# Kernel optimization log

Hardware: AMD Instinct MI355X
Metric: run time of the kernel (lower is better)

Reference implementation:

```python
import jax, jax.numpy as jnp
import numpy as np

EPS = float(np.finfo(np.float32).eps)


def fake_quant_w(w):
    # per-output-channel symmetric int8 fake quant; w: (out, in)
    w_d = jax.lax.stop_gradient(w)
    max_abs = jnp.max(jnp.abs(w_d), axis=1, keepdims=True)
    scale = jnp.maximum(max_abs / 127.0, EPS)
    w_q = jnp.clip(jnp.round(w_d / scale), -127, 127)
    return w_q * scale


def woq_linear(x, w, b):
    return x @ fake_quant_w(w).T + b


def setup_inputs() -> dict:
    key = jax.random.key(0)
    ks = jax.random.split(key, 9)
    dim = 1024
    B, S = 2, 2048
    def wmat(k):
        return jax.random.normal(k, (dim, dim), dtype=jnp.float32) * (1.0 / np.sqrt(dim))
    def bvec(k):
        return jax.random.normal(k, (dim,), dtype=jnp.float32) * 0.01
    return {
        "x": jax.random.normal(ks[0], (B, S, dim), dtype=jnp.float32),
        "wq": wmat(ks[1]), "bq": bvec(ks[2]),
        "wk": wmat(ks[3]), "bk": bvec(ks[4]),
        "wv": wmat(ks[5]), "bv": bvec(ks[6]),
        "wp": wmat(ks[7]), "bp": bvec(ks[8]),
    }


def reference(x, wq, bq, wk, bk, wv, bv, wp, bp):
    B, S, C = x.shape
    H = 16
    D = C // H
    scale = D ** -0.5
    # QKV projections with fake-quantized weights -> (B, H, S, D)
    q = woq_linear(x, wq, bq).reshape(B, S, H, D).transpose(0, 2, 1, 3)
    k = woq_linear(x, wk, bk).reshape(B, S, H, D).transpose(0, 2, 1, 3)
    v = woq_linear(x, wv, bv).reshape(B, S, H, D).transpose(0, 2, 1, 3)
    attn = jnp.einsum("bhsd,bhtd->bhst", q, k) * scale  # (B,H,S,S)
    attn = jax.nn.softmax(attn, axis=-1)
    out = jnp.einsum("bhst,bhtd->bhsd", attn, v)
    out = out.transpose(0, 2, 1, 3).reshape(B, S, C)
    return woq_linear(out, wp, bp)
```

## Files before the change

kernel.cpp:

```cpp
#include <hip/hip_runtime.h>
#include <stdint.h>

typedef short bf16x8 __attribute__((ext_vector_type(8)));
typedef float f32x4 __attribute__((ext_vector_type(4)));
typedef uint16_t u16;
typedef uint32_t u32;
typedef u16 u16x4 __attribute__((ext_vector_type(4)));
typedef u32 u32x4 __attribute__((ext_vector_type(4)));

#define EPSF 1.1920929e-07f

static __device__ __forceinline__ u16 f2bf(float f) {
  union { float f; uint32_t u; } v; v.f = f;
  return (u16)((v.u + 0x7FFFu + ((v.u >> 16) & 1u)) >> 16);
}
static __device__ __forceinline__ float bf2f(u16 h) {
  union { uint32_t u; float f; } v; v.u = ((uint32_t)h) << 16;
  return v.f;
}
static __device__ __forceinline__ float exp2_fast(float x) {
  return __builtin_amdgcn_exp2f(x);
}
static __device__ __forceinline__ u32 cvt_pk_bf16(float lo, float hi) {
  u32 r;
  asm("v_cvt_pk_bf16_f32 %0, %1, %2" : "=v"(r) : "v"(lo), "v"(hi));
  return r;
}
static __device__ __forceinline__ void gload_lds16(const void* g, void* l) {
  __builtin_amdgcn_global_load_lds(
      (const __attribute__((address_space(1))) void*)g,
      (__attribute__((address_space(3))) void*)l, 16, 0, 0);
}
template <int N>
static __device__ __forceinline__ void vmwait() {
  asm volatile("s_waitcnt vmcnt(%0)" ::"i"(N) : "memory");
}

__global__ __launch_bounds__(256) void prep_kernel(
    const float* __restrict__ wq, const float* __restrict__ wk,
    const float* __restrict__ wv, const float* __restrict__ wp,
    const float* __restrict__ x,
    u16* __restrict__ wout, float* __restrict__ scales, u16* __restrict__ xb) {
  const int t = threadIdx.x;
  if (blockIdx.x < 4096) {
    const int row = blockIdx.x & 1023;
    const int mat = blockIdx.x >> 10;
    const float* W = (mat == 0) ? wq : (mat == 1) ? wk : (mat == 2) ? wv : wp;
    const float4 v = ((const float4*)(W + (size_t)row * 1024))[t];
    float m = fmaxf(fmaxf(fabsf(v.x), fabsf(v.y)), fmaxf(fabsf(v.z), fabsf(v.w)));
#pragma unroll
    for (int off = 1; off < 64; off <<= 1) m = fmaxf(m, __shfl_xor(m, off));
    __shared__ float red[4];
    if ((t & 63) == 0) red[t >> 6] = m;
    __syncthreads();
    m = fmaxf(fmaxf(red[0], red[1]), fmaxf(red[2], red[3]));
    const float scale = fmaxf(m / 127.0f, EPSF);
    float q0 = fminf(fmaxf(rintf(v.x / scale), -127.f), 127.f);
    float q1 = fminf(fmaxf(rintf(v.y / scale), -127.f), 127.f);
    float q2 = fminf(fmaxf(rintf(v.z / scale), -127.f), 127.f);
    float q3 = fminf(fmaxf(rintf(v.w / scale), -127.f), 127.f);
    u16x4 o; o.x = f2bf(q0); o.y = f2bf(q1); o.z = f2bf(q2); o.w = f2bf(q3);
    *(u16x4*)(wout + ((size_t)(mat * 1024 + row)) * 1024 + t * 4) = o;
    if (t == 0) scales[mat * 1024 + row] = scale;
  } else {
    const int i = (blockIdx.x - 4096) * 256 + t;
    const float4 v = ((const float4*)x)[i];
    u16x4 hv;
    hv.x = f2bf(v.x); hv.y = f2bf(v.y); hv.z = f2bf(v.z); hv.w = f2bf(v.w);
    *(u16x4*)(xb + (size_t)i * 4) = hv;
  }
}

template <int MODE, int MR, int NR, int NT, int KT, int LDA>
__global__ __launch_bounds__(512) void gemm_kernel(
    const u16* __restrict__ A, const u16* __restrict__ Bw,
    const float* __restrict__ scales, const float* __restrict__ b0,
    const float* __restrict__ b1, const float* __restrict__ b2,
    u16* __restrict__ qkv, float* __restrict__ outp) {
  constexpr int BM = 2 * MR * 16;
  constexpr int BN = 4 * NR * 16;
  constexpr int OPS = BM / 64 + BN / 64;
  __shared__ u16 As[2][BM * 64];
  __shared__ u16 Bs[2][BN * 64];
  const int tid = threadIdx.x;
  const int w = tid >> 6, l = tid & 63;
  const int per = gridDim.x >> 3;
  const int L = (blockIdx.x & 7) * per + (blockIdx.x >> 3);
  const int tile_n = (L % NT) * BN;
  const int tile_m = (L / NT) * BM;
  const int wm = w >> 2, wn = w & 3;
  const int l15 = l & 15, l4 = l >> 4;
  const int sw = l15 & 7;

  f32x4 acc[MR][NR];
  const f32x4 vzero = {0.f, 0.f, 0.f, 0.f};
#pragma unroll
  for (int m = 0; m < MR; ++m)
#pragma unroll
    for (int n = 0; n < NR; ++n) acc[m][n] = vzero;

  const int r8 = tid >> 3;
  const int g = tid & 7;
  const int gs = g ^ (r8 & 7);
  auto STAGE = [&](int slot, int j) {
    const int kb = j * 64;
    const int kbB = kb & 1023;
#pragma unroll
    for (int i = 0; i < BM / 64; ++i)
      gload_lds16(A + (size_t)(tile_m + i * 64 + r8) * LDA + kb + gs * 8,
                  &As[slot][(i * 64 + r8) * 64 + g * 8]);
#pragma unroll
    for (int i = 0; i < BN / 64; ++i)
      gload_lds16(Bw + (size_t)(tile_n + i * 64 + r8) * 1024 + kbB + gs * 8,
                  &Bs[slot][(i * 64 + r8) * 64 + g * 8]);
  };

  STAGE(0, 0);
  STAGE(1, 1);
  vmwait<OPS>();
  __builtin_amdgcn_s_barrier();

  for (int j = 0; j < KT; ++j) {
    const int cur = j & 1;
#pragma unroll
    for (int ks = 0; ks < 2; ++ks) {
      bf16x8 af[MR], bfv[NR];
      const int sg8 = ((ks * 4 + l4) ^ sw) * 8;
#pragma unroll
      for (int m = 0; m < MR; ++m)
        af[m] = *(const bf16x8*)(&As[cur][(wm * (MR * 16) + m * 16 + l15) * 64 + sg8]);
#pragma unroll
      for (int n = 0; n < NR; ++n)
        bfv[n] = *(const bf16x8*)(&Bs[cur][(wn * (NR * 16) + n * 16 + l15) * 64 + sg8]);
      __builtin_amdgcn_s_setprio(1);
#pragma unroll
      for (int m = 0; m < MR; ++m)
#pragma unroll
        for (int n = 0; n < NR; ++n)
          acc[m][n] = __builtin_amdgcn_mfma_f32_16x16x32_bf16(af[m], bfv[n], acc[m][n], 0, 0, 0);
      __builtin_amdgcn_s_setprio(0);
    }
    __builtin_amdgcn_s_barrier();
    if (j + 2 < KT) {
      STAGE(cur, j + 2);
      vmwait<OPS>();
    } else {
      vmwait<0>();
    }
    __builtin_amdgcn_s_barrier();
  }

#pragma unroll
  for (int m = 0; m < MR; ++m) {
#pragma unroll
    for (int n = 0; n < NR; ++n) {
      const int col = tile_n + wn * (NR * 16) + n * 16 + l15;
      const float sc = scales[col];
      if constexpr (MODE == 0) {
        const int mat = col >> 10, oo = col & 1023;
        const float* bias = (mat == 0) ? b0 : (mat == 1) ? b1 : b2;
        const float bb = bias[oo];
        const int hh = oo >> 6, dd = oo & 63;
        if (mat == 2) {
          const int rowm0 = tile_m + wm * (MR * 16) + m * 16 + l4 * 4;
          const int b = rowm0 >> 11, s = rowm0 & 2047;
          u16x4 pk;
#pragma unroll
          for (int jj = 0; jj < 4; ++jj) pk[jj] = f2bf(acc[m][n][jj] * sc + bb);
          const int kpos = (s & ~31) + ((s >> 2) & 3) * 8 + ((s >> 4) & 1) * 4;
          *(u16x4*)(qkv + (size_t)2 * 4194304 +
                    ((size_t)(b * 16 + hh) * 64 + dd) * 2048 + kpos) = pk;
        } else {
#pragma unroll
          for (int jj = 0; jj < 4; ++jj) {
            const int rowm = tile_m + wm * (MR * 16) + m * 16 + l4 * 4 + jj;
            const int b = rowm >> 11, s = rowm & 2047;
            float y = acc[m][n][jj] * sc + bb;
            if (mat == 0) y *= 0.18033688011112042f;
            qkv[(size_t)mat * 4194304 + ((size_t)(b * 16 + hh) * 2048 + s) * 64 + dd] = f2bf(y);
          }
        }
      } else {
        const float bb = b0[col];
#pragma unroll
        for (int jj = 0; jj < 4; ++jj) {
          const int rowm = tile_m + wm * (MR * 16) + m * 16 + l4 * 4 + jj;
          outp[(size_t)rowm * 1024 + col] = acc[m][n][jj] * sc + bb;
        }
      }
    }
  }
}

__global__ __launch_bounds__(512, 4) void attn_kernel(
    const u16* __restrict__ qg, const u16* __restrict__ kg,
    const u16* __restrict__ vtg, u16* __restrict__ po) {
  __shared__ u16 Kt[2][2][64 * 64];
  __shared__ u16 Vt[2][2][64 * 64];
  const int tid = threadIdx.x;
  const int w = tid >> 6, l = tid & 63;
  const int Lb = (blockIdx.x & 7) * 64 + (blockIdx.x >> 3);
  const int bh = Lb >> 4;
  const int qt = Lb & 15;
  const u16* qp = qg + (size_t)bh * 131072;
  const u16* kp = kg + (size_t)bh * 131072;
  const u16* vp = vtg + (size_t)bh * 131072;
  const int wg = w & 3, grp = w >> 2;
  const int qrow0 = qt * 128 + wg * 32;
  const int l15 = l & 15, l4 = l >> 4;
  const int sw = l15 & 7;

  const int sr = tid >> 3, sg = tid & 7;
  const int gsw = (sg ^ (sr & 7)) << 3;
  auto STAGE = [&](const int slot, const int j) {
    const int kA = j * 64, kB = 1024 + j * 64;
    gload_lds16(kp + (size_t)(kA + sr) * 64 + gsw, &Kt[slot][0][tid * 8]);
    gload_lds16(vp + (size_t)sr * 2048 + kA + gsw, &Vt[slot][0][tid * 8]);
    gload_lds16(kp + (size_t)(kB + sr) * 64 + gsw, &Kt[slot][1][tid * 8]);
    gload_lds16(vp + (size_t)sr * 2048 + kB + gsw, &Vt[slot][1][tid * 8]);
  };

  bf16x8 qfr[2][2];
#pragma unroll
  for (int dk = 0; dk < 2; ++dk)
#pragma unroll
    for (int qf = 0; qf < 2; ++qf)
      qfr[dk][qf] =
          *(const bf16x8*)(qp + (size_t)(qrow0 + qf * 16 + l15) * 64 + dk * 32 + l4 * 8);

  const f32x4 vzero = {0.f, 0.f, 0.f, 0.f};
  f32x4 O[4][2];
#pragma unroll
  for (int di = 0; di < 4; ++di)
#pragma unroll
    for (int qf = 0; qf < 2; ++qf) O[di][qf] = vzero;
  float lrun[2] = {0.f, 0.f};

  auto DO_ITER = [&](const int slot, const int j) {
    const u16* Kb = &Kt[slot][grp][0];
    const u16* Vb = &Vt[slot][grp][0];

    f32x4 sfr[2][4];
    {
      bf16x8 kf[4];
#pragma unroll
      for (int ki = 0; ki < 4; ++ki)
        kf[ki] = *(const bf16x8*)(Kb + (ki * 16 + l15) * 64 + ((l4 ^ sw) << 3));
      __builtin_amdgcn_s_setprio(1);
#pragma unroll
      for (int ki = 0; ki < 4; ++ki)
#pragma unroll
        for (int qf = 0; qf < 2; ++qf)
          sfr[qf][ki] = __builtin_amdgcn_mfma_f32_16x16x32_bf16(kf[ki], qfr[0][qf], vzero, 0, 0, 0);
      __builtin_amdgcn_s_setprio(0);
    }
    {
      bf16x8 kf[4];
#pragma unroll
      for (int ki = 0; ki < 4; ++ki)
        kf[ki] = *(const bf16x8*)(Kb + (ki * 16 + l15) * 64 + (((4 + l4) ^ sw) << 3));
      __builtin_amdgcn_s_setprio(1);
#pragma unroll
      for (int ki = 0; ki < 4; ++ki)
#pragma unroll
        for (int qf = 0; qf < 2; ++qf)
          sfr[qf][ki] = __builtin_amdgcn_mfma_f32_16x16x32_bf16(kf[ki], qfr[1][qf], sfr[qf][ki], 0, 0, 0);
      __builtin_amdgcn_s_setprio(0);
    }

    u32 pw[2][8];
#pragma unroll
    for (int qf = 0; qf < 2; ++qf) {
      float rs = 0.f;
#pragma unroll
      for (int ki = 0; ki < 4; ++ki) {
        const f32x4 s4 = sfr[qf][ki];
        const float p0 = exp2_fast(s4[0]);
        const float p1 = exp2_fast(s4[1]);
        const float p2 = exp2_fast(s4[2]);
        const float p3 = exp2_fast(s4[3]);
        rs += (p0 + p1) + (p2 + p3);
        pw[qf][ki * 2 + 0] = cvt_pk_bf16(p0, p1);
        pw[qf][ki * 2 + 1] = cvt_pk_bf16(p2, p3);
      }
      lrun[qf] += rs;
    }

#pragma unroll
    for (int kkl = 0; kkl < 2; ++kkl) {
      const u32x4 t0 = {pw[0][kkl * 4 + 0], pw[0][kkl * 4 + 1],
                        pw[0][kkl * 4 + 2], pw[0][kkl * 4 + 3]};
      const u32x4 t1 = {pw[1][kkl * 4 + 0], pw[1][kkl * 4 + 1],
                        pw[1][kkl * 4 + 2], pw[1][kkl * 4 + 3]};
      const bf16x8 pf0 = __builtin_bit_cast(bf16x8, t0);
      const bf16x8 pf1 = __builtin_bit_cast(bf16x8, t1);
      bf16x8 vf[4];
#pragma unroll
      for (int di = 0; di < 4; ++di)
        vf[di] = *(const bf16x8*)(Vb + (di * 16 + l15) * 64 +
                                  (((kkl * 4 + l4) ^ sw) << 3));
      __builtin_amdgcn_s_setprio(1);
#pragma unroll
      for (int di = 0; di < 4; ++di) {
        O[di][0] = __builtin_amdgcn_mfma_f32_16x16x32_bf16(pf0, vf[di], O[di][0], 0, 0, 0);
        O[di][1] = __builtin_amdgcn_mfma_f32_16x16x32_bf16(pf1, vf[di], O[di][1], 0, 0, 0);
      }
      __builtin_amdgcn_s_setprio(0);
    }

    __builtin_amdgcn_s_barrier();
    if (j + 2 < 16) {
      STAGE(slot, j + 2);
      vmwait<4>();
    } else {
      vmwait<0>();
    }
    __builtin_amdgcn_s_barrier();
  };

  STAGE(0, 0);
  STAGE(1, 1);
  vmwait<4>();
  __builtin_amdgcn_s_barrier();

  for (int jp = 0; jp < 8; ++jp) {
    DO_ITER(0, jp * 2);
    DO_ITER(1, jp * 2 + 1);
  }

  float* Osh = (float*)&Kt[0][0][0];
  float* lsh = (float*)&Vt[0][0][0];
  if (grp == 1) {
    float* ob = Osh + (0 * 4 + wg) * 1024;
#pragma unroll
    for (int di = 0; di < 4; ++di)
#pragma unroll
      for (int jj = 0; jj < 4; ++jj)
        ob[(l4 * 4 + jj) * 64 + di * 16 + l15] = O[di][0][jj];
    lsh[(0 * 4 + wg) * 64 + l] = lrun[0];
  } else {
    float* ob = Osh + (1 * 4 + wg) * 1024;
#pragma unroll
    for (int di = 0; di < 4; ++di)
#pragma unroll
      for (int jj = 0; jj < 4; ++jj)
        ob[(l4 * 4 + jj) * 64 + di * 16 + l15] = O[di][1][jj];
    lsh[(1 * 4 + wg) * 64 + l] = lrun[1];
  }
  __syncthreads();
  const int b = bh >> 4, hh = bh & 15;
  if (grp == 0) {
    const float* obr = Osh + (0 * 4 + wg) * 1024;
    float lt = lrun[0] + lsh[(0 * 4 + wg) * 64 + l];
    lt += __shfl_xor(lt, 16);
    lt += __shfl_xor(lt, 32);
    float lq[4];
#pragma unroll
    for (int jj = 0; jj < 4; ++jj)
      lq[jj] = __builtin_amdgcn_rcpf(__shfl(lt, l4 * 4 + jj));
#pragma unroll
    for (int di = 0; di < 4; ++di)
#pragma unroll
      for (int jj = 0; jj < 4; ++jj) {
        const float oval =
            (O[di][0][jj] + obr[(l4 * 4 + jj) * 64 + di * 16 + l15]) * lq[jj];
        const int srw = qrow0 + l4 * 4 + jj;
        const int c = hh * 64 + di * 16 + l15;
        po[((size_t)(b * 2048 + srw)) * 1024 + c] = f2bf(oval);
      }
  } else {
    const float* obr = Osh + (1 * 4 + wg) * 1024;
    float lt = lrun[1] + lsh[(1 * 4 + wg) * 64 + l];
    lt += __shfl_xor(lt, 16);
    lt += __shfl_xor(lt, 32);
    float lq[4];
#pragma unroll
    for (int jj = 0; jj < 4; ++jj)
      lq[jj] = __builtin_amdgcn_rcpf(__shfl(lt, l4 * 4 + jj));
#pragma unroll
    for (int di = 0; di < 4; ++di)
#pragma unroll
      for (int jj = 0; jj < 4; ++jj) {
        const float oval =
            (O[di][1][jj] + obr[(l4 * 4 + jj) * 64 + di * 16 + l15]) * lq[jj];
        const int srw = qrow0 + 16 + l4 * 4 + jj;
        const int c = hh * 64 + di * 16 + l15;
        po[((size_t)(b * 2048 + srw)) * 1024 + c] = f2bf(oval);
      }
  }
}

extern "C" void kernel_launch(void* const* d_in, const int* in_sizes, int n_in,
                              void* d_out, int out_size, void* d_ws, size_t ws_size,
                              hipStream_t stream) {
  (void)in_sizes; (void)n_in; (void)out_size; (void)ws_size;
  const float* x  = (const float*)d_in[0];
  const float* wq = (const float*)d_in[1];
  const float* bq = (const float*)d_in[2];
  const float* wk = (const float*)d_in[3];
  const float* bk = (const float*)d_in[4];
  const float* wv = (const float*)d_in[5];
  const float* bv = (const float*)d_in[6];
  const float* wp = (const float*)d_in[7];
  const float* bp = (const float*)d_in[8];

  char* ws = (char*)d_ws;
  u16*   wquant = (u16*)ws;
  float* scales = (float*)(ws + 8388608);
  u16*   xb     = (u16*)(ws + 8404992);
  u16*   po     = xb;
  u16*   qkv    = (u16*)(ws + 25182208);

  prep_kernel<<<dim3(8192), dim3(256), 0, stream>>>(
      wq, wk, wv, wp, x, wquant, scales, xb);
  gemm_kernel<0, 4, 3, 16, 16, 1024><<<dim3(512), dim3(512), 0, stream>>>(
      xb, wquant, scales, bq, bk, bv, qkv, nullptr);
  attn_kernel<<<dim3(512), dim3(512), 0, stream>>>(
      qkv, qkv + 4194304, qkv + 8388608, po);
  gemm_kernel<1, 2, 2, 8, 16, 1024><<<dim3(512), dim3(512), 0, stream>>>(
      po, wquant + 3145728, scales + 3072, bp, nullptr, nullptr, nullptr, (float*)d_out);
}
```

Measured before the change: 96.08 us.

## Add dedicated QKV GEMM kernel with 256x192 tiles and split-phase MFMA scheduling

Replaces the templated QKV projection GEMM (128x192 tiles, 512 blocks) with a dedicated kernel using 256x192 tiles and 256 blocks, so each block reuses more staged data per K step. The inner loop splits each k-substep into two halves with barriers and priority hints around MFMA bursts, and unrolls the double-buffer slots. Fewer blocks than CUs (256 on mi355x) and higher register pressure from 24 accumulators per wave may lower occupancy and leave hardware idle.

```diff
diff --git a/kernel.cpp b/kernel.cpp
--- a/kernel.cpp
+++ b/kernel.cpp
@@ -71,12 +71,126 @@
   }
 }
 
-template <int MODE, int MR, int NR, int NT, int KT, int LDA>
+__global__ __launch_bounds__(512, 2) void qkv_kernel(
+    const u16* __restrict__ A, const u16* __restrict__ Bw,
+    const float* __restrict__ scales, const float* __restrict__ b0,
+    const float* __restrict__ b1, const float* __restrict__ b2,
+    u16* __restrict__ qkv) {
+  __shared__ u16 As[2][256 * 64];
+  __shared__ u16 Bs[2][192 * 64];
+  const int tid = threadIdx.x;
+  const int w = tid >> 6, l = tid & 63;
+  const int L = (blockIdx.x & 7) * 32 + (blockIdx.x >> 3);
+  const int tile_n = (L & 15) * 192;
+  const int tile_m = (L >> 4) * 256;
+  const int wm = w >> 2, wn = w & 3;
+  const int l15 = l & 15, l4 = l >> 4;
+  const int sw = l15 & 7;
+
+  f32x4 acc[8][3];
+  const f32x4 vzero = {0.f, 0.f, 0.f, 0.f};
+#pragma unroll
+  for (int m = 0; m < 8; ++m)
+#pragma unroll
+    for (int n = 0; n < 3; ++n) acc[m][n] = vzero;
+
+  const int r8 = tid >> 3, g = tid & 7;
+  const int gs = g ^ (r8 & 7);
+  auto STAGE = [&](const int slot, const int j) {
+    const int kb = j * 64;
+#pragma unroll
+    for (int i = 0; i < 4; ++i)
+      gload_lds16(A + (size_t)(tile_m + i * 64 + r8) * 1024 + kb + gs * 8,
+                  &As[slot][(i * 64 + r8) * 64 + g * 8]);
+#pragma unroll
+    for (int i = 0; i < 3; ++i)
+      gload_lds16(Bw + (size_t)(tile_n + i * 64 + r8) * 1024 + kb + gs * 8,
+                  &Bs[slot][(i * 64 + r8) * 64 + g * 8]);
+  };
+
+  STAGE(0, 0);
+  STAGE(1, 1);
+  vmwait<7>();
+  __builtin_amdgcn_s_barrier();
+
+  auto KSTEP = [&](const int s, const int j) {
+#pragma unroll
+    for (int ks = 0; ks < 2; ++ks) {
+      bf16x8 bfv[3];
+      const int sg8 = ((ks * 4 + l4) ^ sw) << 3;
+#pragma unroll
+      for (int n = 0; n < 3; ++n)
+        bfv[n] = *(const bf16x8*)(&Bs[s][(wn * 48 + n * 16 + l15) * 64 + sg8]);
+#pragma unroll
+      for (int mh = 0; mh < 2; ++mh) {
+        bf16x8 af[4];
+#pragma unroll
+        for (int m4 = 0; m4 < 4; ++m4)
+          af[m4] = *(const bf16x8*)(&As[s][(wm * 128 + mh * 64 + m4 * 16 + l15) * 64 + sg8]);
+        __builtin_amdgcn_s_barrier();
+        __builtin_amdgcn_s_setprio(1);
+#pragma unroll
+        for (int m4 = 0; m4 < 4; ++m4)
+#pragma unroll
+          for (int n = 0; n < 3; ++n)
+            acc[mh * 4 + m4][n] = __builtin_amdgcn_mfma_f32_16x16x32_bf16(
+                af[m4], bfv[n], acc[mh * 4 + m4][n], 0, 0, 0);
+        __builtin_amdgcn_s_setprio(0);
+        __builtin_amdgcn_s_barrier();
+      }
+    }
+    if (j + 2 < 16) {
+      STAGE(s, j + 2);
+      vmwait<7>();
+    } else {
+      vmwait<0>();
+    }
+    __builtin_amdgcn_s_barrier();
+  };
+
+  for (int jp = 0; jp < 8; ++jp) {
+    KSTEP(0, jp * 2);
+    KSTEP(1, jp * 2 + 1);
+  }
+
+#pragma unroll
+  for (int m = 0; m < 8; ++m) {
+#pragma unroll
+    for (int n = 0; n < 3; ++n) {
+      const int col = tile_n + wn * 48 + n * 16 + l15;
+      const float sc = scales[col];
+      const int mat = col >> 10, oo = col & 1023;
+      const float* bias = (mat == 0) ? b0 : (mat == 1) ? b1 : b2;
+      const float bb = bias[oo];
+      const int hh = oo >> 6, dd = oo & 63;
+      if (mat == 2) {
+        const int rowm0 = tile_m + wm * 128 + m * 16 + l4 * 4;
+        const int b = rowm0 >> 11, s = rowm0 & 2047;
+        u16x4 pk;
+#pragma unroll
+        for (int jj = 0; jj < 4; ++jj) pk[jj] = f2bf(acc[m][n][jj] * sc + bb);
+        const int kpos = (s & ~31) + ((s >> 2) & 3) * 8 + ((s >> 4) & 1) * 4;
+        *(u16x4*)(qkv + (size_t)2 * 4194304 +
+                  ((size_t)(b * 16 + hh) * 64 + dd) * 2048 + kpos) = pk;
+      } else {
+#pragma unroll
+        for (int jj = 0; jj < 4; ++jj) {
+          const int rowm = tile_m + wm * 128 + m * 16 + l4 * 4 + jj;
+          const int b = rowm >> 11, s = rowm & 2047;
+          float y = acc[m][n][jj] * sc + bb;
+          if (mat == 0) y *= 0.18033688011112042f;
+          qkv[(size_t)mat * 4194304 + ((size_t)(b * 16 + hh) * 2048 + s) * 64 + dd] = f2bf(y);
+        }
+      }
+    }
+  }
+}
+
+template <int MR, int NR, int NT, int KT, int LDA>
 __global__ __launch_bounds__(512) void gemm_kernel(
     const u16* __restrict__ A, const u16* __restrict__ Bw,
     const float* __restrict__ scales, const float* __restrict__ b0,
-    const float* __restrict__ b1, const float* __restrict__ b2,
-    u16* __restrict__ qkv, float* __restrict__ outp) {
+    float* __restrict__ outp) {
   constexpr int BM = 2 * MR * 16;
   constexpr int BN = 4 * NR * 16;
   constexpr int OPS = BM / 64 + BN / 64;
@@ -156,37 +270,11 @@
     for (int n = 0; n < NR; ++n) {
       const int col = tile_n + wn * (NR * 16) + n * 16 + l15;
       const float sc = scales[col];
-      if constexpr (MODE == 0) {
-        const int mat = col >> 10, oo = col & 1023;
-        const float* bias = (mat == 0) ? b0 : (mat == 1) ? b1 : b2;
-        const float bb = bias[oo];
-        const int hh = oo >> 6, dd = oo & 63;
-        if (mat == 2) {
-          const int rowm0 = tile_m + wm * (MR * 16) + m * 16 + l4 * 4;
-          const int b = rowm0 >> 11, s = rowm0 & 2047;
-          u16x4 pk;
-#pragma unroll
-          for (int jj = 0; jj < 4; ++jj) pk[jj] = f2bf(acc[m][n][jj] * sc + bb);
-          const int kpos = (s & ~31) + ((s >> 2) & 3) * 8 + ((s >> 4) & 1) * 4;
-          *(u16x4*)(qkv + (size_t)2 * 4194304 +
-                    ((size_t)(b * 16 + hh) * 64 + dd) * 2048 + kpos) = pk;
-        } else {
-#pragma unroll
-          for (int jj = 0; jj < 4; ++jj) {
-            const int rowm = tile_m + wm * (MR * 16) + m * 16 + l4 * 4 + jj;
-            const int b = rowm >> 11, s = rowm & 2047;
-            float y = acc[m][n][jj] * sc + bb;
-            if (mat == 0) y *= 0.18033688011112042f;
-            qkv[(size_t)mat * 4194304 + ((size_t)(b * 16 + hh) * 2048 + s) * 64 + dd] = f2bf(y);
-          }
-        }
-      } else {
-        const float bb = b0[col];
-#pragma unroll
-        for (int jj = 0; jj < 4; ++jj) {
-          const int rowm = tile_m + wm * (MR * 16) + m * 16 + l4 * 4 + jj;
-          outp[(size_t)rowm * 1024 + col] = acc[m][n][jj] * sc + bb;
-        }
+      const float bb = b0[col];
+#pragma unroll
+      for (int jj = 0; jj < 4; ++jj) {
+        const int rowm = tile_m + wm * (MR * 16) + m * 16 + l4 * 4 + jj;
+        outp[(size_t)rowm * 1024 + col] = acc[m][n][jj] * sc + bb;
       }
     }
   }
@@ -413,10 +501,10 @@
 
   prep_kernel<<<dim3(8192), dim3(256), 0, stream>>>(
       wq, wk, wv, wp, x, wquant, scales, xb);
-  gemm_kernel<0, 4, 3, 16, 16, 1024><<<dim3(512), dim3(512), 0, stream>>>(
-      xb, wquant, scales, bq, bk, bv, qkv, nullptr);
+  qkv_kernel<<<dim3(256), dim3(512), 0, stream>>>(
+      xb, wquant, scales, bq, bk, bv, qkv);
   attn_kernel<<<dim3(512), dim3(512), 0, stream>>>(
       qkv, qkv + 4194304, qkv + 8388608, po);
-  gemm_kernel<1, 2, 2, 8, 16, 1024><<<dim3(512), dim3(512), 0, stream>>>(
-      po, wquant + 3145728, scales + 3072, bp, nullptr, nullptr, nullptr, (float*)d_out);
-}
+  gemm_kernel<2, 2, 8, 16, 1024><<<dim3(512), dim3(512), 0, stream>>>(
+      po, wquant + 3145728, scales + 3072, bp, (float*)d_out);
+}
```

New measurement: 103.1 us. 7.3% more time.
